# Performance work log

Measured on AMD Instinct MI355X. Metric: run time of the kernel, lower is better.

## Reference

```python
import jax, jax.numpy as jnp
import numpy as np

# ---- HashGrid config (tcnn defaults from module __init__) ----
N_LEVELS = 6
F = 2                      # n_features_per_level
T = 2 ** 19                # hashmap size
BASE = 16                  # base_resolution, per_level_scale=2.0
_RES = [BASE * (2 ** l) for l in range(N_LEVELS)]          # 16..512
_SIZES = [min(r ** 3, T) for r in _RES]                    # dense if grid fits
_OFFSETS = [0] + list(np.cumsum(_SIZES))
TOTAL_ENTRIES = int(_OFFSETS[-1])
_PRIMES = (1, 2654435761, 805459861)
BOX_R = 1.0
DIM_H = 64
DIM_IN = 3 + N_LEVELS * F


def hash_encode(xn, grid):
    """Multi-res hash-grid encoding. xn: [N,3] in [0,1]; grid: [TOTAL_ENTRIES, F]."""
    feats = []
    for l in range(N_LEVELS):
        res, size, off = _RES[l], _SIZES[l], _OFFSETS[l]
        dense = (res ** 3) <= T
        pos = xn * jnp.float32(res - 1) + 0.5          # tcnn: scale*x + 0.5
        pg = jnp.floor(pos)
        frac = pos - pg                                # [N,3]
        pgi = pg.astype(jnp.uint32)
        acc = jnp.zeros((xn.shape[0], F), xn.dtype)
        for corner in range(8):                        # trilinear, 8 corners
            cb = jnp.array([(corner >> d) & 1 for d in range(3)], dtype=jnp.uint32)
            c = pgi + cb                               # [N,3] corner coords
            w = jnp.prod(jnp.where(cb == 1, frac, 1.0 - frac), axis=-1)  # [N]
            if dense:
                c = jnp.minimum(c, jnp.uint32(res - 1))
                idx = c[:, 0] + c[:, 1] * jnp.uint32(res) + c[:, 2] * jnp.uint32(res * res)
            else:
                idx = ((c[:, 0] * jnp.uint32(_PRIMES[0]))
                       ^ (c[:, 1] * jnp.uint32(_PRIMES[1]))
                       ^ (c[:, 2] * jnp.uint32(_PRIMES[2]))) % jnp.uint32(size)
            acc = acc + w[:, None] * grid[jnp.uint32(off) + idx]
        feats.append(acc)
    return jnp.concatenate(feats, axis=-1)             # [N, 12]


def setup_inputs() -> dict:
    key = jax.random.key(0)
    k0, k1, k2 = jax.random.split(key, 3)
    N = 2_097_152
    x = jax.random.uniform(k0, (N, 3), jnp.float32, -1.0, 1.0)
    grid = jax.random.uniform(k1, (TOTAL_ENTRIES, F), jnp.float32, -1e-2, 1e-2)
    W0 = jax.random.normal(k2, (DIM_IN, DIM_H), jnp.float32) * float(np.sqrt(2.0 / DIM_H))
    b0 = jnp.zeros((DIM_H,), jnp.float32)
    W1 = jnp.full((DIM_H, 1), float(np.sqrt(np.pi / DIM_H)), jnp.float32)
    b1 = jnp.full((1,), -1.0, jnp.float32)             # -init_radius
    return {"x": x, "grid": grid, "W0": W0, "b0": b0, "W1": W1, "b1": b1}


def reference(x, grid, W0, b0, W1, b1):
    xn = (x + BOX_R) / (2.0 * BOX_R)                   # normalize to [0,1]
    f = hash_encode(xn, grid)                          # [N,12]
    h = jnp.concatenate([x, f], axis=-1)               # [N,15]
    h = jax.nn.relu(h @ W0 + b0)                       # [N,64]
    return h @ W1 + b1                                 # [N,1] scalar level s
```

## Files before the change

kernel.cpp:

```cpp
#include <hip/hip_runtime.h>


static __device__ __forceinline__ unsigned umin_(unsigned a, unsigned b) {
    return a < b ? a : b;
}

#define HP1 2654435761u
#define HP2 805459861u
#define HMASK ((1u << 19) - 1u)

__global__ __launch_bounds__(256) void hash_level_kernel(
    const float* __restrict__ x,
    const float2* __restrict__ tab,
    float2* __restrict__ feat,
    float scale, int N)
{
    const int gid = blockIdx.x * 256 + threadIdx.x;
    if (gid >= N) return;

    const float px = __builtin_nontemporal_load(x + 3 * gid + 0);
    const float py = __builtin_nontemporal_load(x + 3 * gid + 1);
    const float pz = __builtin_nontemporal_load(x + 3 * gid + 2);

    const float p0 = fmaf((px + 1.0f) * 0.5f, scale, 0.5f);
    const float p1 = fmaf((py + 1.0f) * 0.5f, scale, 0.5f);
    const float p2 = fmaf((pz + 1.0f) * 0.5f, scale, 0.5f);
    const float g0 = floorf(p0), g1 = floorf(p1), g2 = floorf(p2);
    const float f0 = p0 - g0, f1 = p1 - g1, f2 = p2 - g2;
    const unsigned i0 = (unsigned)g0, i1 = (unsigned)g1, i2 = (unsigned)g2;

    const float wx[2] = {1.0f - f0, f0};
    const float wy[2] = {1.0f - f1, f1};
    const float wz[2] = {1.0f - f2, f2};
    const unsigned hx[2] = {i0, i0 + 1u};
    const unsigned hy[2] = {i1 * HP1, (i1 + 1u) * HP1};
    const unsigned hz[2] = {i2 * HP2, (i2 + 1u) * HP2};

    unsigned idx[8];
    float w[8];
    #pragma unroll
    for (int c = 0; c < 8; ++c) {
        const int bx = c & 1, by = (c >> 1) & 1, bz = (c >> 2) & 1;
        idx[c] = (hx[bx] ^ hy[by] ^ hz[bz]) & HMASK;
        w[c] = wx[bx] * wy[by] * wz[bz];
    }
    float2 v[8];
    #pragma unroll
    for (int c = 0; c < 8; ++c) v[c] = tab[idx[c]];

    float a0 = 0.0f, a1 = 0.0f;
    #pragma unroll
    for (int c = 0; c < 8; ++c) {
        a0 = fmaf(w[c], v[c].x, a0);
        a1 = fmaf(w[c], v[c].y, a1);
    }
    float* fp = (float*)(feat + gid);
    __builtin_nontemporal_store(a0, fp + 0);
    __builtin_nontemporal_store(a1, fp + 1);
}

__global__ __launch_bounds__(256) void dense_mlp_kernel(
    const float* __restrict__ x,
    const float* __restrict__ grid,
    const float2* __restrict__ feat,
    const float* __restrict__ W0,
    const float* __restrict__ b0,
    const float* __restrict__ W1,
    const float* __restrict__ b1,
    float* __restrict__ out, int N)
{
    __shared__ float sW0T[64 * 16];
    __shared__ float sW1[64];

    const int tid = threadIdx.x;
    for (int t = tid; t < 960; t += 256) {
        int j = t / 15;
        int i = t - j * 15;
        sW0T[j * 16 + i] = W0[i * 64 + j];
    }
    if (tid < 64) {
        sW0T[tid * 16 + 15] = b0[tid];
        sW1[tid] = W1[tid];
    }
    __syncthreads();

    const int gid = blockIdx.x * 256 + tid;
    if (gid >= N) return;

    const float px = __builtin_nontemporal_load(x + 3 * gid + 0);
    const float py = __builtin_nontemporal_load(x + 3 * gid + 1);
    const float pz = __builtin_nontemporal_load(x + 3 * gid + 2);
    const float xn0 = (px + 1.0f) * 0.5f;
    const float xn1 = (py + 1.0f) * 0.5f;
    const float xn2 = (pz + 1.0f) * 0.5f;

    float h[16];
    h[0] = px; h[1] = py; h[2] = pz;
    h[15] = 1.0f;

    const float2* gtab = (const float2*)grid;

    constexpr int      RES[3] = {16, 32, 64};
    constexpr unsigned OFF[3] = {0u, 4096u, 36864u};

    #pragma unroll
    for (int l = 0; l < 3; ++l) {
        const float scale = (float)(RES[l] - 1);
        const float p0 = fmaf(xn0, scale, 0.5f);
        const float p1 = fmaf(xn1, scale, 0.5f);
        const float p2 = fmaf(xn2, scale, 0.5f);
        const float g0 = floorf(p0), g1 = floorf(p1), g2 = floorf(p2);
        const float f0 = p0 - g0, f1 = p1 - g1, f2 = p2 - g2;
        const unsigned i0 = (unsigned)g0, i1 = (unsigned)g1, i2 = (unsigned)g2;

        const float wx[2] = {1.0f - f0, f0};
        const float wy[2] = {1.0f - f1, f1};
        const float wz[2] = {1.0f - f2, f2};

        const unsigned rm1 = (unsigned)(RES[l] - 1);
        const unsigned res = (unsigned)RES[l];
        const unsigned cx[2] = {umin_(i0, rm1), umin_(i0 + 1u, rm1)};
        const unsigned cy[2] = {umin_(i1, rm1) * res, umin_(i1 + 1u, rm1) * res};
        const unsigned cz[2] = {umin_(i2, rm1) * res * res,
                                umin_(i2 + 1u, rm1) * res * res};

        float a0 = 0.0f, a1 = 0.0f;
        #pragma unroll
        for (int c = 0; c < 8; ++c) {
            const int bx = c & 1, by = (c >> 1) & 1, bz = (c >> 2) & 1;
            const unsigned idx = cx[bx] + cy[by] + cz[bz];
            const float w = wx[bx] * wy[by] * wz[bz];
            const float2 v = gtab[OFF[l] + idx];
            a0 = fmaf(w, v.x, a0);
            a1 = fmaf(w, v.y, a1);
        }
        h[3 + 2 * l] = a0;
        h[4 + 2 * l] = a1;
    }

    #pragma unroll
    for (int l = 0; l < 3; ++l) {
        const float* fp = (const float*)(feat + (size_t)l * N + gid);
        h[9 + 2 * l]  = __builtin_nontemporal_load(fp + 0);
        h[10 + 2 * l] = __builtin_nontemporal_load(fp + 1);
    }

    float o = b1[0];
    #pragma unroll 8
    for (int j = 0; j < 64; ++j) {
        float s = 0.0f;
        #pragma unroll
        for (int i = 0; i < 16; ++i)
            s = fmaf(h[i], sW0T[j * 16 + i], s);
        s = fmaxf(s, 0.0f);
        o = fmaf(s, sW1[j], o);
    }
    __builtin_nontemporal_store(o, out + gid);
}

extern "C" void kernel_launch(void* const* d_in, const int* in_sizes, int n_in,
                              void* d_out, int out_size, void* d_ws, size_t ws_size,
                              hipStream_t stream) {
    const float* x    = (const float*)d_in[0];
    const float* grid = (const float*)d_in[1];
    const float* W0   = (const float*)d_in[2];
    const float* b0   = (const float*)d_in[3];
    const float* W1   = (const float*)d_in[4];
    const float* b1   = (const float*)d_in[5];
    float* out = (float*)d_out;

    const int N = in_sizes[0] / 3;
    const int blocks = (N + 255) / 256;

    const float2* gtab = (const float2*)grid;
    float2* feat = (float2*)d_ws;

    hash_level_kernel<<<blocks, 256, 0, stream>>>(x, gtab + 299008u,
                                                  feat + (size_t)0 * N, 127.0f, N);
    hash_level_kernel<<<blocks, 256, 0, stream>>>(x, gtab + 823296u,
                                                  feat + (size_t)1 * N, 255.0f, N);
    hash_level_kernel<<<blocks, 256, 0, stream>>>(x, gtab + 1347584u,
                                                  feat + (size_t)2 * N, 511.0f, N);
    dense_mlp_kernel<<<blocks, 256, 0, stream>>>(x, grid, feat, W0, b0, W1, b1,
                                                 out, N);
}
```

Measured before the change: 357.9 us.

## Store hash features as packed bf16 and batch four points per MLP thread

The intermediate hash-level features are stored as packed bf16 pairs, which halves the workspace write and read traffic between the hash kernels and the MLP kernel. The MLP kernel now handles four points per thread, so each weight row it loads is reused across four points. Weights are pre-transposed by a small prep kernel into global memory and read as uniform loads, replacing the per-block shared-memory setup and barrier. This adds bf16 rounding error on half of the features and more register pressure from the launch-bounds occupancy hint.

```diff
diff --git a/kernel.cpp b/kernel.cpp
--- a/kernel.cpp
+++ b/kernel.cpp
@@ -1,18 +1,42 @@
 #include <hip/hip_runtime.h>
 
-
-static __device__ __forceinline__ unsigned umin_(unsigned a, unsigned b) {
-    return a < b ? a : b;
-}
 
 #define HP1 2654435761u
 #define HP2 805459861u
 #define HMASK ((1u << 19) - 1u)
 
+static __device__ __forceinline__ unsigned umin_(unsigned a, unsigned b) {
+    return a < b ? a : b;
+}
+
+static __device__ __forceinline__ unsigned f2bf(float f) {
+    unsigned u = __float_as_uint(f);
+    return (u + 0x7fffu + ((u >> 16) & 1u)) >> 16;
+}
+static __device__ __forceinline__ float bf2f_lo(unsigned p) {
+    return __uint_as_float((p & 0xffffu) << 16);
+}
+static __device__ __forceinline__ float bf2f_hi(unsigned p) {
+    return __uint_as_float(p & 0xffff0000u);
+}
+
+__global__ __launch_bounds__(256) void prep_kernel(
+    const float* __restrict__ W0, const float* __restrict__ b0,
+    const float* __restrict__ W1, const float* __restrict__ b1,
+    float* __restrict__ wt)
+{
+    for (int t = threadIdx.x; t < 1024; t += 256) {
+        const int j = t >> 4, i = t & 15;
+        wt[t] = (i == 15) ? b0[j] : W0[i * 64 + j];
+    }
+    if (threadIdx.x < 64) wt[1024 + threadIdx.x] = W1[threadIdx.x];
+    if (threadIdx.x == 0) wt[1088] = b1[0];
+}
+
 __global__ __launch_bounds__(256) void hash_level_kernel(
     const float* __restrict__ x,
     const float2* __restrict__ tab,
-    float2* __restrict__ feat,
+    unsigned* __restrict__ feat,
     float scale, int N)
 {
     const int gid = blockIdx.x * 256 + threadIdx.x;
@@ -54,108 +78,111 @@
         a0 = fmaf(w[c], v[c].x, a0);
         a1 = fmaf(w[c], v[c].y, a1);
     }
-    float* fp = (float*)(feat + gid);
-    __builtin_nontemporal_store(a0, fp + 0);
-    __builtin_nontemporal_store(a1, fp + 1);
-}
-
-__global__ __launch_bounds__(256) void dense_mlp_kernel(
+    __builtin_nontemporal_store(f2bf(a0) | (f2bf(a1) << 16), feat + gid);
+}
+
+static __device__ __forceinline__ void dense_level(
+    const float2* __restrict__ tab, unsigned res,
+    float xn0, float xn1, float xn2, float& o0, float& o1)
+{
+    const float scale = (float)(res - 1);
+    const float p0 = fmaf(xn0, scale, 0.5f);
+    const float p1 = fmaf(xn1, scale, 0.5f);
+    const float p2 = fmaf(xn2, scale, 0.5f);
+    const float g0 = floorf(p0), g1 = floorf(p1), g2 = floorf(p2);
+    const float f0 = p0 - g0, f1 = p1 - g1, f2 = p2 - g2;
+    const unsigned i0 = (unsigned)g0, i1 = (unsigned)g1, i2 = (unsigned)g2;
+
+    const unsigned rm1 = res - 1u;
+    const unsigned cx[2] = {umin_(i0, rm1), umin_(i0 + 1u, rm1)};
+    const unsigned cy[2] = {umin_(i1, rm1) * res, umin_(i1 + 1u, rm1) * res};
+    const unsigned cz[2] = {umin_(i2, rm1) * res * res,
+                            umin_(i2 + 1u, rm1) * res * res};
+    const float wx[2] = {1.0f - f0, f0};
+    const float wy[2] = {1.0f - f1, f1};
+    const float wz[2] = {1.0f - f2, f2};
+
+    float a0 = 0.0f, a1 = 0.0f;
+    #pragma unroll
+    for (int c = 0; c < 8; ++c) {
+        const int bx = c & 1, by = (c >> 1) & 1, bz = (c >> 2) & 1;
+        const unsigned idx = cx[bx] + cy[by] + cz[bz];
+        const float w = wx[bx] * wy[by] * wz[bz];
+        const float2 v = tab[idx];
+        a0 = fmaf(w, v.x, a0);
+        a1 = fmaf(w, v.y, a1);
+    }
+    o0 = a0;
+    o1 = a1;
+}
+
+__global__ __launch_bounds__(256, 4) void dense_mlp_kernel(
     const float* __restrict__ x,
     const float* __restrict__ grid,
-    const float2* __restrict__ feat,
-    const float* __restrict__ W0,
-    const float* __restrict__ b0,
-    const float* __restrict__ W1,
-    const float* __restrict__ b1,
+    const unsigned* __restrict__ feat,
+    const float* __restrict__ wt,
     float* __restrict__ out, int N)
 {
-    __shared__ float sW0T[64 * 16];
-    __shared__ float sW1[64];
-
     const int tid = threadIdx.x;
-    for (int t = tid; t < 960; t += 256) {
-        int j = t / 15;
-        int i = t - j * 15;
-        sW0T[j * 16 + i] = W0[i * 64 + j];
-    }
-    if (tid < 64) {
-        sW0T[tid * 16 + 15] = b0[tid];
-        sW1[tid] = W1[tid];
-    }
-    __syncthreads();
-
-    const int gid = blockIdx.x * 256 + tid;
-    if (gid >= N) return;
-
-    const float px = __builtin_nontemporal_load(x + 3 * gid + 0);
-    const float py = __builtin_nontemporal_load(x + 3 * gid + 1);
-    const float pz = __builtin_nontemporal_load(x + 3 * gid + 2);
-    const float xn0 = (px + 1.0f) * 0.5f;
-    const float xn1 = (py + 1.0f) * 0.5f;
-    const float xn2 = (pz + 1.0f) * 0.5f;
-
-    float h[16];
-    h[0] = px; h[1] = py; h[2] = pz;
-    h[15] = 1.0f;
-
+    const int base = blockIdx.x * 1024 + tid;
     const float2* gtab = (const float2*)grid;
 
-    constexpr int      RES[3] = {16, 32, 64};
-    constexpr unsigned OFF[3] = {0u, 4096u, 36864u};
-
-    #pragma unroll
-    for (int l = 0; l < 3; ++l) {
-        const float scale = (float)(RES[l] - 1);
-        const float p0 = fmaf(xn0, scale, 0.5f);
-        const float p1 = fmaf(xn1, scale, 0.5f);
-        const float p2 = fmaf(xn2, scale, 0.5f);
-        const float g0 = floorf(p0), g1 = floorf(p1), g2 = floorf(p2);
-        const float f0 = p0 - g0, f1 = p1 - g1, f2 = p2 - g2;
-        const unsigned i0 = (unsigned)g0, i1 = (unsigned)g1, i2 = (unsigned)g2;
-
-        const float wx[2] = {1.0f - f0, f0};
-        const float wy[2] = {1.0f - f1, f1};
-        const float wz[2] = {1.0f - f2, f2};
-
-        const unsigned rm1 = (unsigned)(RES[l] - 1);
-        const unsigned res = (unsigned)RES[l];
-        const unsigned cx[2] = {umin_(i0, rm1), umin_(i0 + 1u, rm1)};
-        const unsigned cy[2] = {umin_(i1, rm1) * res, umin_(i1 + 1u, rm1) * res};
-        const unsigned cz[2] = {umin_(i2, rm1) * res * res,
-                                umin_(i2 + 1u, rm1) * res * res};
-
-        float a0 = 0.0f, a1 = 0.0f;
+    float h[4][16];
+
+    #pragma unroll
+    for (int k = 0; k < 4; ++k) {
+        const int g = base + 256 * k;
+        const int gs = (g < N) ? g : 0;
+
+        const float px = __builtin_nontemporal_load(x + 3 * gs + 0);
+        const float py = __builtin_nontemporal_load(x + 3 * gs + 1);
+        const float pz = __builtin_nontemporal_load(x + 3 * gs + 2);
+        const float xn0 = (px + 1.0f) * 0.5f;
+        const float xn1 = (py + 1.0f) * 0.5f;
+        const float xn2 = (pz + 1.0f) * 0.5f;
+
+        h[k][0] = px; h[k][1] = py; h[k][2] = pz;
+        h[k][15] = 1.0f;
+
+        dense_level(gtab + 0u,     16u, xn0, xn1, xn2, h[k][3], h[k][4]);
+        dense_level(gtab + 4096u,  32u, xn0, xn1, xn2, h[k][5], h[k][6]);
+        dense_level(gtab + 36864u, 64u, xn0, xn1, xn2, h[k][7], h[k][8]);
+
         #pragma unroll
-        for (int c = 0; c < 8; ++c) {
-            const int bx = c & 1, by = (c >> 1) & 1, bz = (c >> 2) & 1;
-            const unsigned idx = cx[bx] + cy[by] + cz[bz];
-            const float w = wx[bx] * wy[by] * wz[bz];
-            const float2 v = gtab[OFF[l] + idx];
-            a0 = fmaf(w, v.x, a0);
-            a1 = fmaf(w, v.y, a1);
+        for (int l = 0; l < 3; ++l) {
+            const unsigned p = __builtin_nontemporal_load(
+                feat + (size_t)l * N + gs);
+            h[k][9 + 2 * l]  = bf2f_lo(p);
+            h[k][10 + 2 * l] = bf2f_hi(p);
         }
-        h[3 + 2 * l] = a0;
-        h[4 + 2 * l] = a1;
-    }
-
-    #pragma unroll
-    for (int l = 0; l < 3; ++l) {
-        const float* fp = (const float*)(feat + (size_t)l * N + gid);
-        h[9 + 2 * l]  = __builtin_nontemporal_load(fp + 0);
-        h[10 + 2 * l] = __builtin_nontemporal_load(fp + 1);
-    }
-
-    float o = b1[0];
-    #pragma unroll 8
+    }
+
+    const float b1v = wt[1088];
+    float o[4] = {b1v, b1v, b1v, b1v};
+
+    #pragma unroll 4
     for (int j = 0; j < 64; ++j) {
-        float s = 0.0f;
+        float r[16];
         #pragma unroll
         for (int i = 0; i < 16; ++i)
-            s = fmaf(h[i], sW0T[j * 16 + i], s);
-        s = fmaxf(s, 0.0f);
-        o = fmaf(s, sW1[j], o);
-    }
-    __builtin_nontemporal_store(o, out + gid);
+            r[i] = wt[j * 16 + i];
+        const float w1j = wt[1024 + j];
+        #pragma unroll
+        for (int k = 0; k < 4; ++k) {
+            float s = 0.0f;
+            #pragma unroll
+            for (int i = 0; i < 16; ++i)
+                s = fmaf(h[k][i], r[i], s);
+            s = fmaxf(s, 0.0f);
+            o[k] = fmaf(s, w1j, o[k]);
+        }
+    }
+
+    #pragma unroll
+    for (int k = 0; k < 4; ++k) {
+        const int g = base + 256 * k;
+        if (g < N) __builtin_nontemporal_store(o[k], out + g);
+    }
 }
 
 extern "C" void kernel_launch(void* const* d_in, const int* in_sizes, int n_in,
@@ -170,17 +197,21 @@
     float* out = (float*)d_out;
 
     const int N = in_sizes[0] / 3;
-    const int blocks = (N + 255) / 256;
+    const int blocks1 = (N + 255) / 256;
+    const int blocks4 = (N + 1023) / 1024;
 
     const float2* gtab = (const float2*)grid;
-    float2* feat = (float2*)d_ws;
-
-    hash_level_kernel<<<blocks, 256, 0, stream>>>(x, gtab + 299008u,
-                                                  feat + (size_t)0 * N, 127.0f, N);
-    hash_level_kernel<<<blocks, 256, 0, stream>>>(x, gtab + 823296u,
-                                                  feat + (size_t)1 * N, 255.0f, N);
-    hash_level_kernel<<<blocks, 256, 0, stream>>>(x, gtab + 1347584u,
-                                                  feat + (size_t)2 * N, 511.0f, N);
-    dense_mlp_kernel<<<blocks, 256, 0, stream>>>(x, grid, feat, W0, b0, W1, b1,
-                                                 out, N);
-}
+    unsigned* feat = (unsigned*)d_ws;
+    const size_t feat_bytes = ((size_t)3 * N * 4 + 255) & ~(size_t)255;
+    float* wt = (float*)((char*)d_ws + feat_bytes);
+
+    prep_kernel<<<1, 256, 0, stream>>>(W0, b0, W1, b1, wt);
+
+    hash_level_kernel<<<blocks1, 256, 0, stream>>>(x, gtab + 299008u,
+                                                   feat + (size_t)0 * N, 127.0f, N);
+    hash_level_kernel<<<blocks1, 256, 0, stream>>>(x, gtab + 823296u,
+                                                   feat + (size_t)1 * N, 255.0f, N);
+    hash_level_kernel<<<blocks1, 256, 0, stream>>>(x, gtab + 1347584u,
+                                                   feat + (size_t)2 * N, 511.0f, N);
+    dense_mlp_kernel<<<blocks4, 256, 0, stream>>>(x, grid, feat, wt, out, N);
+}
```

Measured after the change: 370.9 us. 3.6% more time.
